# Kernel tuning notes

Hardware: AMD Instinct MI355X
Metric: run time of the kernel (lower is better)

Reference implementation:

```python
import jax, jax.numpy as jnp
import numpy as np


def _conv(h_src, w_e, src, dst, n_dst):
    # u_mul_e('x','w','m') then sum('m','y'): gather src feats, scale by edge weight, segment-sum into dst
    m = h_src[src] * w_e[:, None]  # [E, F]
    return jax.ops.segment_sum(m, dst, num_segments=n_dst)


def setup_inputs() -> dict:
    key = jax.random.key(0)
    ks = jax.random.split(key, 12)
    in_feats, n_hidden, n_classes = 256, 256, 47
    n0, n1, n2, n3 = 100000, 50000, 25000, 12500
    e1, e2, e3 = 800000, 400000, 200000

    def edges(k, e, n_src, n_dst):
        k1, k2, k3 = jax.random.split(k, 3)
        return (jax.random.randint(k1, (e,), 0, n_src, dtype=jnp.int32),
                jax.random.randint(k2, (e,), 0, n_dst, dtype=jnp.int32),
                jax.random.normal(k3, (e,), jnp.float32))

    x = jax.random.normal(ks[0], (n0, in_feats), jnp.float32)
    s1, d1, ew1 = edges(ks[1], e1, n0, n1)
    s2, d2, ew2 = edges(ks[2], e2, n1, n2)
    s3, d3, ew3 = edges(ks[3], e3, n2, n3)
    W1 = jax.random.normal(ks[4], (in_feats, n_hidden), jnp.float32) / np.float32(np.sqrt(in_feats))
    b1 = jnp.zeros((n_hidden,), jnp.float32)
    W2 = jax.random.normal(ks[5], (n_hidden, n_hidden), jnp.float32) / np.float32(np.sqrt(n_hidden))
    b2 = jnp.zeros((n_hidden,), jnp.float32)
    W3 = jax.random.normal(ks[6], (n_hidden, n_classes), jnp.float32) / np.float32(np.sqrt(n_hidden))
    b3 = jnp.zeros((n_classes,), jnp.float32)
    u_sum = jax.random.normal(ks[7], (n2,), jnp.float32)  # per-src-node scalar on last block
    return dict(x=x, W1=W1, b1=b1, W2=W2, b2=b2, W3=W3, b3=b3,
                ew1=ew1, ew2=ew2, ew3=ew3, u_sum=u_sum,
                s1=s1, d1=d1, s2=s2, d2=d2, s3=s3, d3=d3,
                n1=n1, n2=n2, n3=n3)


def reference(x, W1, b1, W2, b2, W3, b3, ew1, ew2, ew3, u_sum,
              s1, d1, s2, d2, s3, d3, n1, n2, n3):
    # layer 1: GraphConv + relu
    h = x @ W1 + b1
    y = jax.nn.relu(_conv(h, ew1, s1, d1, n1))
    # layer 2: GraphConv + relu
    h = y @ W2 + b2
    y = jax.nn.relu(_conv(h, ew2, s2, d2, n2))
    # layer 3: GraphConvReg (no relu on last layer)
    h = y @ W3 + b3  # src feats of last block, [n2, n_classes]
    y = _conv(h, ew3, s3, d3, n3)  # [n3, n_classes]
    mean_x = jnp.mean(y, axis=0)  # [n_classes]
    mean_u = u_sum / jnp.asarray(n3, h.dtype)  # [n2]
    diff = mean_u[:, None] * h - mean_x
    reg_loss = jnp.sum(diff * diff) / (h.shape[0] * h.shape[1])
    return (y, reg_loss)
```

## Files before the change

### kernel.cpp

```cpp
#include <hip/hip_runtime.h>

typedef unsigned int uint;
typedef __attribute__((ext_vector_type(8))) short bf16x8;
typedef __attribute__((ext_vector_type(4))) float f32x4;

__device__ __forceinline__ float b2f(ushort h) { return __uint_as_float(((uint)h) << 16); }
__device__ __forceinline__ ushort f2b(float f) {
    uint u = __float_as_uint(f);
    return (ushort)((u + 0x7fffu + ((u >> 16) & 1u)) >> 16);
}

__global__ __launch_bounds__(256) void zero_i(int* __restrict__ p, int n) {
    int i = blockIdx.x * 256 + threadIdx.x;
    int st = gridDim.x * 256;
    for (; i < n; i += st) p[i] = 0;
}

__global__ __launch_bounds__(1024) void prep_k(
    const float* __restrict__ x, ushort* __restrict__ xb, long n8,
    const float* __restrict__ W1, const float* __restrict__ W2,
    const float* __restrict__ W3, const float* __restrict__ b3,
    ushort* __restrict__ Wt1, ushort* __restrict__ Wt2,
    ushort* __restrict__ Wt3, float* __restrict__ b3p, int NC,
    const int* __restrict__ d1, const int* __restrict__ d2, const int* __restrict__ d3,
    int E1, int E2, int E3, int n1, int n2,
    int* __restrict__ cnt, int* __restrict__ slot, int Gf2b, int NSLOT) {
    int b = blockIdx.x;
    if (b < Gf2b) {
        long i = (long)b * 1024 + threadIdx.x;
        long st = (long)Gf2b * 1024;
        for (; i < n8; i += st) {
            float4 a = reinterpret_cast<const float4*>(x)[i * 2];
            float4 c = reinterpret_cast<const float4*>(x)[i * 2 + 1];
            ushort4 o0, o1;
            o0.x = f2b(a.x); o0.y = f2b(a.y); o0.z = f2b(a.z); o0.w = f2b(a.w);
            o1.x = f2b(c.x); o1.y = f2b(c.y); o1.z = f2b(c.z); o1.w = f2b(c.w);
            reinterpret_cast<ushort4*>(xb)[i * 2] = o0;
            reinterpret_cast<ushort4*>(xb)[i * 2 + 1] = o1;
        }
        return;
    }
    b -= Gf2b;
    if (b < 256) {
        int k = b;
        int t = threadIdx.x;
        if (t < 256) {
            Wt1[(long)t * 256 + k] = f2b(W1[(long)k * 256 + t]);
        } else if (t < 512) {
            int n = t - 256;
            Wt2[(long)n * 256 + k] = f2b(W2[(long)k * 256 + n]);
        } else if (t < 640) {
            int n = t - 512;
            float v = (n < NC) ? W3[(long)k * NC + n] : 0.f;
            Wt3[(long)n * 256 + k] = f2b(v);
            if (k == 0) b3p[n] = (n < NC) ? b3[n] : 0.f;
        }
        return;
    }
    b -= 256;
    const int tid0 = b * 1024 + threadIdx.x;
    const int st = NSLOT * 1024;
    {
        int n4 = E1 >> 2;
        const int4* dd = (const int4*)d1;
        for (int i = tid0; i < n4; i += st) {
            int4 v = dd[i];
            slot[i * 4 + 0] = atomicAdd(&cnt[v.x], 1);
            slot[i * 4 + 1] = atomicAdd(&cnt[v.y], 1);
            slot[i * 4 + 2] = atomicAdd(&cnt[v.z], 1);
            slot[i * 4 + 3] = atomicAdd(&cnt[v.w], 1);
        }
        for (int i = n4 * 4 + tid0; i < E1; i += st) slot[i] = atomicAdd(&cnt[d1[i]], 1);
    }
    {
        int n4 = E2 >> 2;
        const int4* dd = (const int4*)d2;
        int* sl = slot + E1;
        for (int i = tid0; i < n4; i += st) {
            int4 v = dd[i];
            sl[i * 4 + 0] = atomicAdd(&cnt[n1 + v.x], 1);
            sl[i * 4 + 1] = atomicAdd(&cnt[n1 + v.y], 1);
            sl[i * 4 + 2] = atomicAdd(&cnt[n1 + v.z], 1);
            sl[i * 4 + 3] = atomicAdd(&cnt[n1 + v.w], 1);
        }
        for (int i = n4 * 4 + tid0; i < E2; i += st) sl[i] = atomicAdd(&cnt[n1 + d2[i]], 1);
    }
    {
        int n4 = E3 >> 2;
        const int4* dd = (const int4*)d3;
        int* sl = slot + E1 + E2;
        int base = n1 + n2;
        for (int i = tid0; i < n4; i += st) {
            int4 v = dd[i];
            sl[i * 4 + 0] = atomicAdd(&cnt[base + v.x], 1);
            sl[i * 4 + 1] = atomicAdd(&cnt[base + v.y], 1);
            sl[i * 4 + 2] = atomicAdd(&cnt[base + v.z], 1);
            sl[i * 4 + 3] = atomicAdd(&cnt[base + v.w], 1);
        }
        for (int i = n4 * 4 + tid0; i < E3; i += st) sl[i] = atomicAdd(&cnt[base + d3[i]], 1);
    }
}

__global__ __launch_bounds__(1024) void scan1(const int* __restrict__ cnt, int* __restrict__ off,
                                              int* __restrict__ bsum, int n) {
    __shared__ int wsum[16];
    const int lane = threadIdx.x & 63;
    const int wid = threadIdx.x >> 6;
    int i = blockIdx.x * 1024 + threadIdx.x;
    int v = (i < n) ? cnt[i] : 0;
    int s = v;
    #pragma unroll
    for (int o = 1; o < 64; o <<= 1) {
        int t = __shfl_up(s, o, 64);
        if (lane >= o) s += t;
    }
    if (lane == 63) wsum[wid] = s;
    __syncthreads();
    if (wid == 0 && lane < 16) {
        int t = wsum[lane];
        #pragma unroll
        for (int o = 1; o < 16; o <<= 1) {
            int u = __shfl_up(t, o, 64);
            if (lane >= o) t += u;
        }
        wsum[lane] = t;
    }
    __syncthreads();
    int woff = (wid > 0) ? wsum[wid - 1] : 0;
    if (i < n) off[i] = woff + s - v;
    if (threadIdx.x == 0) bsum[blockIdx.x] = wsum[15];
}

__global__ __launch_bounds__(128) void scan2(const int* __restrict__ bsum, int* __restrict__ bbase,
                                             int nb, int* __restrict__ off_end, float* __restrict__ acc) {
    __shared__ int w0tot;
    int tid = threadIdx.x;
    int lane = tid & 63;
    int wid = tid >> 6;
    int v = (tid < nb) ? bsum[tid] : 0;
    int s = v;
    #pragma unroll
    for (int o = 1; o < 64; o <<= 1) {
        int t = __shfl_up(s, o, 64);
        if (lane >= o) s += t;
    }
    if (wid == 0 && lane == 63) w0tot = s;
    __syncthreads();
    int base = (wid == 1) ? w0tot : 0;
    if (tid < nb) bbase[tid] = base + s - v;
    if (tid == nb - 1) *off_end = base + s;
    if (tid == 0) *acc = 0.f;
}

__global__ __launch_bounds__(256) void scan3(int* __restrict__ off, const int* __restrict__ bbase, int n) {
    int i = blockIdx.x * 256 + threadIdx.x;
    int st = gridDim.x * 256;
    for (; i < n; i += st) off[i] += bbase[i >> 10];
}

__global__ __launch_bounds__(256) void place_k(
    const int* __restrict__ s1, const int* __restrict__ d1,
    const int* __restrict__ s2, const int* __restrict__ d2,
    const int* __restrict__ s3, const int* __restrict__ d3,
    const float* __restrict__ w1, const float* __restrict__ w2, const float* __restrict__ w3,
    const int* __restrict__ slot, const int* __restrict__ off,
    int2* __restrict__ csr, int E1, int E2, int E3, int n1, int n2) {
    const int tid0 = blockIdx.x * 256 + threadIdx.x;
    const int st = gridDim.x * 256;
    {
        int n4 = E1 >> 2;
        for (int i = tid0; i < n4; i += st) {
            int4 dv = ((const int4*)d1)[i];
            int4 sv = ((const int4*)s1)[i];
            int4 pv = ((const int4*)slot)[i];
            float4 wv = ((const float4*)w1)[i];
            csr[off[dv.x] + pv.x] = make_int2(sv.x, __float_as_int(wv.x));
            csr[off[dv.y] + pv.y] = make_int2(sv.y, __float_as_int(wv.y));
            csr[off[dv.z] + pv.z] = make_int2(sv.z, __float_as_int(wv.z));
            csr[off[dv.w] + pv.w] = make_int2(sv.w, __float_as_int(wv.w));
        }
        for (int i = n4 * 4 + tid0; i < E1; i += st)
            csr[off[d1[i]] + slot[i]] = make_int2(s1[i], __float_as_int(w1[i]));
    }
    {
        int n4 = E2 >> 2;
        const int* sl = slot + E1;
        for (int i = tid0; i < n4; i += st) {
            int4 dv = ((const int4*)d2)[i];
            int4 sv = ((const int4*)s2)[i];
            int4 pv = ((const int4*)sl)[i];
            float4 wv = ((const float4*)w2)[i];
            csr[off[n1 + dv.x] + pv.x] = make_int2(sv.x, __float_as_int(wv.x));
            csr[off[n1 + dv.y] + pv.y] = make_int2(sv.y, __float_as_int(wv.y));
            csr[off[n1 + dv.z] + pv.z] = make_int2(sv.z, __float_as_int(wv.z));
            csr[off[n1 + dv.w] + pv.w] = make_int2(sv.w, __float_as_int(wv.w));
        }
        for (int i = n4 * 4 + tid0; i < E2; i += st)
            csr[off[n1 + d2[i]] + sl[i]] = make_int2(s2[i], __float_as_int(w2[i]));
    }
    {
        int n4 = E3 >> 2;
        const int* sl = slot + E1 + E2;
        int base = n1 + n2;
        for (int i = tid0; i < n4; i += st) {
            int4 dv = ((const int4*)d3)[i];
            int4 sv = ((const int4*)s3)[i];
            int4 pv = ((const int4*)sl)[i];
            float4 wv = ((const float4*)w3)[i];
            csr[off[base + dv.x] + pv.x] = make_int2(sv.x, __float_as_int(wv.x));
            csr[off[base + dv.y] + pv.y] = make_int2(sv.y, __float_as_int(wv.y));
            csr[off[base + dv.z] + pv.z] = make_int2(sv.z, __float_as_int(wv.z));
            csr[off[base + dv.w] + pv.w] = make_int2(sv.w, __float_as_int(wv.w));
        }
        for (int i = n4 * 4 + tid0; i < E3; i += st)
            csr[off[base + d3[i]] + sl[i]] = make_int2(s3[i], __float_as_int(w3[i]));
    }
}

__global__ __launch_bounds__(256) void gather_b4(const ushort* __restrict__ hb,
                                                 const int* __restrict__ off,
                                                 const int2* __restrict__ csr,
                                                 ushort* __restrict__ out,
                                                 float* __restrict__ rw, int n_dst) {
    int d = blockIdx.x * 4 + (threadIdx.x >> 6);
    if (d >= n_dst) return;
    int lane = threadIdx.x & 63;
    int i0 = off[d], i1 = off[d + 1];
    float a0 = 0.f, a1 = 0.f, a2 = 0.f, a3 = 0.f, sw = 0.f;
    for (int base = i0; base < i1; base += 64) {
        int cnt = i1 - base;
        if (cnt > 64) cnt = 64;
        int2 e = csr[base + (lane < cnt ? lane : 0)];
        int j = 0;
        for (; j + 8 <= cnt; j += 8) {
            int s[8]; float wv[8];
            #pragma unroll
            for (int u = 0; u < 8; ++u) {
                s[u] = __shfl(e.x, j + u, 64);
                wv[u] = __int_as_float(__shfl(e.y, j + u, 64));
            }
            ushort4 v[8];
            #pragma unroll
            for (int u = 0; u < 8; ++u)
                v[u] = *reinterpret_cast<const ushort4*>(&hb[(long)s[u] * 256 + lane * 4]);
            #pragma unroll
            for (int u = 0; u < 8; ++u) {
                a0 += wv[u] * b2f(v[u].x);
                a1 += wv[u] * b2f(v[u].y);
                a2 += wv[u] * b2f(v[u].z);
                a3 += wv[u] * b2f(v[u].w);
                sw += wv[u];
            }
        }
        for (; j < cnt; ++j) {
            int sv = __shfl(e.x, j, 64);
            float wv = __int_as_float(__shfl(e.y, j, 64));
            ushort4 v = *reinterpret_cast<const ushort4*>(&hb[(long)sv * 256 + lane * 4]);
            a0 += wv * b2f(v.x); a1 += wv * b2f(v.y); a2 += wv * b2f(v.z); a3 += wv * b2f(v.w);
            sw += wv;
        }
    }
    ushort4 o;
    o.x = f2b(a0); o.y = f2b(a1); o.z = f2b(a2); o.w = f2b(a3);
    *reinterpret_cast<ushort4*>(&out[(long)d * 256 + lane * 4]) = o;
    if (lane == 0) rw[d] = sw;
}

__global__ __launch_bounds__(256) void gather_small(const float* __restrict__ h,
                                                    const int* __restrict__ off,
                                                    const int2* __restrict__ csr,
                                                    float* __restrict__ y, int n_dst, int F) {
    int d = blockIdx.x * 4 + (threadIdx.x >> 6);
    if (d >= n_dst) return;
    int lane = threadIdx.x & 63;
    int i0 = off[d], i1 = off[d + 1];
    float acc = 0.f;
    for (int base = i0; base < i1; base += 64) {
        int cnt = i1 - base;
        if (cnt > 64) cnt = 64;
        int2 e = csr[base + (lane < cnt ? lane : 0)];
        int j = 0;
        for (; j + 4 <= cnt; j += 4) {
            int s[4]; float wv[4];
            #pragma unroll
            for (int u = 0; u < 4; ++u) {
                s[u] = __shfl(e.x, j + u, 64);
                wv[u] = __int_as_float(__shfl(e.y, j + u, 64));
            }
            float v[4];
            #pragma unroll
            for (int u = 0; u < 4; ++u) v[u] = (lane < F) ? h[(long)s[u] * F + lane] : 0.f;
            #pragma unroll
            for (int u = 0; u < 4; ++u) acc += wv[u] * v[u];
        }
        for (; j < cnt; ++j) {
            int sv = __shfl(e.x, j, 64);
            float wv = __int_as_float(__shfl(e.y, j, 64));
            if (lane < F) acc += wv * h[(long)sv * F + lane];
        }
    }
    if (lane < F) y[(long)d * F + lane] = acc;
}

template <bool RELU, bool OUTF32, bool ROWSC, bool GUARDN>
__global__ __launch_bounds__(256) void gemm_mfma(const ushort* __restrict__ A,
                                                 const ushort* __restrict__ Bt,
                                                 const float* __restrict__ bias,
                                                 const float* __restrict__ rowsc,
                                                 ushort* __restrict__ Cb,
                                                 float* __restrict__ Cf,
                                                 int M, int Nout, int K) {
    __shared__ ushort As[4096];
    __shared__ ushort Bs[4096];
    const int tid = threadIdx.x;
    const int w = tid >> 6;
    const int lane = tid & 63;
    const int l15 = lane & 15;
    const int l4 = lane >> 4;
    const int bm = blockIdx.x * 128;
    const int bn = blockIdx.y * 128;
    const int wm = w >> 1, wn = w & 1;

    int ra0 = bm + w * 16 + l15;       if (ra0 >= M) ra0 = M - 1;
    int ra1 = bm + (w + 4) * 16 + l15; if (ra1 >= M) ra1 = M - 1;
    const ushort* pa0 = A + (long)ra0 * K + l4 * 8;
    const ushort* pa1 = A + (long)ra1 * K + l4 * 8;
    const ushort* pb0 = Bt + (long)(bn + w * 16 + l15) * K + l4 * 8;
    const ushort* pb1 = Bt + (long)(bn + (w + 4) * 16 + l15) * K + l4 * 8;

    f32x4 acc[4][4];
    f32x4 zz = {0.f, 0.f, 0.f, 0.f};
    #pragma unroll
    for (int m = 0; m < 4; ++m)
        #pragma unroll
        for (int n = 0; n < 4; ++n) acc[m][n] = zz;

    for (int k0 = 0; k0 < K; k0 += 32) {
        __builtin_amdgcn_global_load_lds((const __attribute__((address_space(1))) void*)pa0,
                                         (__attribute__((address_space(3))) void*)&As[w * 512], 16, 0, 0);
        __builtin_amdgcn_global_load_lds((const __attribute__((address_space(1))) void*)pa1,
                                         (__attribute__((address_space(3))) void*)&As[(w + 4) * 512], 16, 0, 0);
        __builtin_amdgcn_global_load_lds((const __attribute__((address_space(1))) void*)pb0,
                                         (__attribute__((address_space(3))) void*)&Bs[w * 512], 16, 0, 0);
        __builtin_amdgcn_global_load_lds((const __attribute__((address_space(1))) void*)pb1,
                                         (__attribute__((address_space(3))) void*)&Bs[(w + 4) * 512], 16, 0, 0);
        pa0 += 32; pa1 += 32; pb0 += 32; pb1 += 32;
        __syncthreads();
        bf16x8 af[4], bfr[4];
        #pragma unroll
        for (int m = 0; m < 4; ++m)
            af[m] = *reinterpret_cast<const bf16x8*>(&As[(wm * 4 + m) * 512 + lane * 8]);
        #pragma unroll
        for (int n = 0; n < 4; ++n)
            bfr[n] = *reinterpret_cast<const bf16x8*>(&Bs[(wn * 4 + n) * 512 + lane * 8]);
        #pragma unroll
        for (int m = 0; m < 4; ++m)
            #pragma unroll
            for (int n = 0; n < 4; ++n)
                acc[m][n] = __builtin_amdgcn_mfma_f32_16x16x32_bf16(af[m], bfr[n], acc[m][n], 0, 0, 0);
        __syncthreads();
    }

    const int rbase = bm + wm * 64;
    const int cbase = bn + wn * 64;
    #pragma unroll
    for (int m = 0; m < 4; ++m) {
        #pragma unroll
        for (int q = 0; q < 4; ++q) {
            int r = rbase + m * 16 + l4 * 4 + q;
            if (r >= M) continue;
            float rs = ROWSC ? rowsc[r] : 1.f;
            #pragma unroll
            for (int n = 0; n < 4; ++n) {
                int c = cbase + n * 16 + l15;
                float v = acc[m][n][q] + rs * bias[c];
                if (RELU) v = fmaxf(v, 0.f);
                if (!GUARDN || c < Nout) {
                    if (OUTF32) Cf[(long)r * Nout + c] = v;
                    else Cb[(long)r * Nout + c] = f2b(v);
                }
            }
        }
    }
}

__global__ __launch_bounds__(256) void col_mean(const float* __restrict__ y,
                                                float* __restrict__ mean_x,
                                                int rows, int cols) {
    int j = blockIdx.x;
    float s = 0.f;
    for (int i = threadIdx.x; i < rows; i += blockDim.x) s += y[(long)i * cols + j];
    __shared__ float red[256];
    red[threadIdx.x] = s;
    __syncthreads();
    for (int o = 128; o > 0; o >>= 1) {
        if (threadIdx.x < o) red[threadIdx.x] += red[threadIdx.x + o];
        __syncthreads();
    }
    if (threadIdx.x == 0) mean_x[j] = red[0] / (float)rows;
}

__global__ __launch_bounds__(256) void reg_loss_k(const float* __restrict__ h,
                                                  const float* __restrict__ u_sum,
                                                  const float* __restrict__ mean_x,
                                                  float* __restrict__ acc,
                                                  int rows, int cols, float inv_n3) {
    long total = (long)rows * cols;
    long idx = (long)blockIdx.x * blockDim.x + threadIdx.x;
    long stride = (long)gridDim.x * blockDim.x;
    float s = 0.f;
    for (long t = idx; t < total; t += stride) {
        int i = (int)(t / cols);
        int j = (int)(t - (long)i * cols);
        float mu = u_sum[i] * inv_n3;
        float d = mu * h[t] - mean_x[j];
        s += d * d;
    }
    __shared__ float red[256];
    red[threadIdx.x] = s;
    __syncthreads();
    for (int o = 128; o > 0; o >>= 1) {
        if (threadIdx.x < o) red[threadIdx.x] += red[threadIdx.x + o];
        __syncthreads();
    }
    if (threadIdx.x == 0) atomicAdd(acc, red[0]);
}

__global__ void finalize_k(float* __restrict__ out, const float* __restrict__ acc, float scale) {
    if (threadIdx.x == 0) *out = *acc * scale;
}

extern "C" void kernel_launch(void* const* d_in, const int* in_sizes, int n_in,
                              void* d_out, int out_size, void* d_ws, size_t ws_size,
                              hipStream_t stream) {
    const float* x   = (const float*)d_in[0];
    const float* W1  = (const float*)d_in[1];
    const float* b1  = (const float*)d_in[2];
    const float* W2  = (const float*)d_in[3];
    const float* b2  = (const float*)d_in[4];
    const float* W3  = (const float*)d_in[5];
    const float* b3  = (const float*)d_in[6];
    const float* ew1 = (const float*)d_in[7];
    const float* ew2 = (const float*)d_in[8];
    const float* ew3 = (const float*)d_in[9];
    const float* u_sum = (const float*)d_in[10];
    const int* s1 = (const int*)d_in[11];
    const int* d1 = (const int*)d_in[12];
    const int* s2 = (const int*)d_in[13];
    const int* d2 = (const int*)d_in[14];
    const int* s3 = (const int*)d_in[15];
    const int* d3 = (const int*)d_in[16];

    const int K  = 256;
    const int n0 = in_sizes[0] / K;
    const int E1 = in_sizes[7];
    const int E2 = in_sizes[8];
    const int E3 = in_sizes[9];
    const int n2 = in_sizes[10];
    const int NC = in_sizes[5] / K;
    const int n3 = (out_size - 1) / NC;
    const int n1 = 50000;

    const int NT = n1 + n2 + n3;
    const int Et = E1 + E2 + E3;
    const int nb = (NT + 1023) / 1024;
    const int Gf2b = 1024;
    const int NSLOT = 2048;

    float* ws = (float*)d_ws;
    long o = 0;
    auto take = [&](long words) { float* p = ws + o; o += (words + 3) & ~3L; return p; };
    int*    off  = (int*)take(NT + 1);
    int*    cnt  = (int*)take(NT);
    float*  rw   = take(n1 + n2);
    int*    bsum = (int*)take(nb);
    int*    bbase= (int*)take(nb);
    int*    slot = (int*)take(Et);
    int2*   csr  = (int2*)take(2L * Et);
    ushort* Wt1b = (ushort*)take(256 * 256 / 2);
    ushort* Wt2b = (ushort*)take(256 * 256 / 2);
    ushort* Wt3b = (ushort*)take(128 * 256 / 2);
    float*  b3p  = take(128);
    ushort* aggb = (ushort*)take((long)n1 * 256 / 2);
    ushort* xb   = (ushort*)take((long)n0 * 256 / 2);
    float*  h3   = take((long)n2 * NC);
    float*  mean_x = take(64);
    float*  accs   = take(4);

    ushort* y1b = xb;
    ushort* y2b = xb + (long)n1 * 256;
    float*  rw1 = rw;
    float*  rw2 = rw + n1;

    float* y3   = (float*)d_out;
    float* loss = y3 + (long)n3 * NC;

    dim3 blk(256);

    zero_i<<<dim3(128), blk, 0, stream>>>(cnt, NT);
    prep_k<<<dim3(Gf2b + 256 + NSLOT), dim3(1024), 0, stream>>>(
        x, xb, (long)n0 * 256 / 8,
        W1, W2, W3, b3, Wt1b, Wt2b, Wt3b, b3p, NC,
        d1, d2, d3, E1, E2, E3, n1, n2, cnt, slot, Gf2b, NSLOT);

    scan1<<<dim3(nb), dim3(1024), 0, stream>>>(cnt, off, bsum, NT);
    scan2<<<dim3(1), dim3(128), 0, stream>>>(bsum, bbase, nb, &off[NT], accs);
    scan3<<<dim3(128), blk, 0, stream>>>(off, bbase, NT);
    place_k<<<dim3(2048), blk, 0, stream>>>(s1, d1, s2, d2, s3, d3, ew1, ew2, ew3,
                                            slot, off, csr, E1, E2, E3, n1, n2);

    gather_b4<<<dim3((n1 + 3) / 4), blk, 0, stream>>>(xb, off, csr, aggb, rw1, n1);
    gemm_mfma<true, false, true, false><<<dim3((n1 + 127) / 128, 2), blk, 0, stream>>>(
        aggb, Wt1b, b1, rw1, y1b, nullptr, n1, 256, K);

    gather_b4<<<dim3((n2 + 3) / 4), blk, 0, stream>>>(y1b, off + n1, csr, aggb, rw2, n2);
    gemm_mfma<true, false, true, false><<<dim3((n2 + 127) / 128, 2), blk, 0, stream>>>(
        aggb, Wt2b, b2, rw2, y2b, nullptr, n2, 256, K);

    gemm_mfma<false, true, false, true><<<dim3((n2 + 127) / 128, 1), blk, 0, stream>>>(
        y2b, Wt3b, b3p, nullptr, nullptr, h3, n2, NC, K);
    gather_small<<<dim3((n3 + 3) / 4), blk, 0, stream>>>(h3, off + n1 + n2, csr, y3, n3, NC);

    col_mean<<<dim3(NC), blk, 0, stream>>>(y3, mean_x, n3, NC);
    reg_loss_k<<<dim3(512), blk, 0, stream>>>(h3, u_sum, mean_x, accs, n2, NC, 1.0f / (float)n3);
    finalize_k<<<dim3(1), dim3(1), 0, stream>>>(loss, accs, 1.0f / ((float)n2 * (float)NC));
}
```

Before: 347.3 us.

## Replace global-atomic CSR build with two-pass LDS bucket sort by destination

The old path counted edges per destination with global atomics and then scattered them into CSR order. The new path is a two-level counting sort. Each block first builds a shared-memory histogram over 64-node buckets, the per-block counts are scanned, edges are scattered into bucket order, and each bucket is then sorted locally to produce offsets and CSR entries. This removes contended global atomics and the zeroing kernel, at the cost of an extra pass and an extra temporary buffer. It also adds a 4-way unrolled tail loop to the bf16 gather.

```diff
diff --git a/kernel.cpp b/kernel.cpp
--- a/kernel.cpp
+++ b/kernel.cpp
@@ -10,11 +10,7 @@
     return (ushort)((u + 0x7fffu + ((u >> 16) & 1u)) >> 16);
 }
 
-__global__ __launch_bounds__(256) void zero_i(int* __restrict__ p, int n) {
-    int i = blockIdx.x * 256 + threadIdx.x;
-    int st = gridDim.x * 256;
-    for (; i < n; i += st) p[i] = 0;
-}
+#define NBLK_S 256
 
 __global__ __launch_bounds__(1024) void prep_k(
     const float* __restrict__ x, ushort* __restrict__ xb, long n8,
@@ -24,7 +20,8 @@
     ushort* __restrict__ Wt3, float* __restrict__ b3p, int NC,
     const int* __restrict__ d1, const int* __restrict__ d2, const int* __restrict__ d3,
     int E1, int E2, int E3, int n1, int n2,
-    int* __restrict__ cnt, int* __restrict__ slot, int Gf2b, int NSLOT) {
+    int* __restrict__ bh, int NBKT, int chunk, int Gf2b) {
+    __shared__ int hist[2048];
     int b = blockIdx.x;
     if (b < Gf2b) {
         long i = (long)b * 1024 + threadIdx.x;
@@ -58,47 +55,20 @@
         return;
     }
     b -= 256;
-    const int tid0 = b * 1024 + threadIdx.x;
-    const int st = NSLOT * 1024;
-    {
-        int n4 = E1 >> 2;
-        const int4* dd = (const int4*)d1;
-        for (int i = tid0; i < n4; i += st) {
-            int4 v = dd[i];
-            slot[i * 4 + 0] = atomicAdd(&cnt[v.x], 1);
-            slot[i * 4 + 1] = atomicAdd(&cnt[v.y], 1);
-            slot[i * 4 + 2] = atomicAdd(&cnt[v.z], 1);
-            slot[i * 4 + 3] = atomicAdd(&cnt[v.w], 1);
-        }
-        for (int i = n4 * 4 + tid0; i < E1; i += st) slot[i] = atomicAdd(&cnt[d1[i]], 1);
-    }
-    {
-        int n4 = E2 >> 2;
-        const int4* dd = (const int4*)d2;
-        int* sl = slot + E1;
-        for (int i = tid0; i < n4; i += st) {
-            int4 v = dd[i];
-            sl[i * 4 + 0] = atomicAdd(&cnt[n1 + v.x], 1);
-            sl[i * 4 + 1] = atomicAdd(&cnt[n1 + v.y], 1);
-            sl[i * 4 + 2] = atomicAdd(&cnt[n1 + v.z], 1);
-            sl[i * 4 + 3] = atomicAdd(&cnt[n1 + v.w], 1);
-        }
-        for (int i = n4 * 4 + tid0; i < E2; i += st) sl[i] = atomicAdd(&cnt[n1 + d2[i]], 1);
-    }
-    {
-        int n4 = E3 >> 2;
-        const int4* dd = (const int4*)d3;
-        int* sl = slot + E1 + E2;
-        int base = n1 + n2;
-        for (int i = tid0; i < n4; i += st) {
-            int4 v = dd[i];
-            sl[i * 4 + 0] = atomicAdd(&cnt[base + v.x], 1);
-            sl[i * 4 + 1] = atomicAdd(&cnt[base + v.y], 1);
-            sl[i * 4 + 2] = atomicAdd(&cnt[base + v.z], 1);
-            sl[i * 4 + 3] = atomicAdd(&cnt[base + v.w], 1);
-        }
-        for (int i = n4 * 4 + tid0; i < E3; i += st) sl[i] = atomicAdd(&cnt[base + d3[i]], 1);
-    }
+    const int Et = E1 + E2 + E3;
+    const int c0 = b * chunk;
+    const int c1 = (c0 + chunk < Et) ? c0 + chunk : Et;
+    for (int i = threadIdx.x; i < NBKT; i += 1024) hist[i] = 0;
+    __syncthreads();
+    for (int i = c0 + (int)threadIdx.x; i < c1; i += 1024) {
+        int g;
+        if (i < E1) g = d1[i];
+        else if (i < E1 + E2) g = n1 + d2[i - E1];
+        else g = n1 + n2 + d3[i - E1 - E2];
+        atomicAdd(&hist[g >> 6], 1);
+    }
+    __syncthreads();
+    for (int k = threadIdx.x; k < NBKT; k += 1024) bh[k * NBLK_S + b] = hist[k];
 }
 
 __global__ __launch_bounds__(1024) void scan1(const int* __restrict__ cnt, int* __restrict__ off,
@@ -131,89 +101,103 @@
     if (threadIdx.x == 0) bsum[blockIdx.x] = wsum[15];
 }
 
-__global__ __launch_bounds__(128) void scan2(const int* __restrict__ bsum, int* __restrict__ bbase,
-                                             int nb, int* __restrict__ off_end, float* __restrict__ acc) {
-    __shared__ int w0tot;
+__global__ __launch_bounds__(1024) void scan2b(const int* __restrict__ bsum, int* __restrict__ bbase,
+                                               int n, int* __restrict__ offNT, float* __restrict__ acc) {
+    __shared__ int wsum[16];
     int tid = threadIdx.x;
     int lane = tid & 63;
     int wid = tid >> 6;
-    int v = (tid < nb) ? bsum[tid] : 0;
+    int v = (tid < n) ? bsum[tid] : 0;
     int s = v;
     #pragma unroll
     for (int o = 1; o < 64; o <<= 1) {
         int t = __shfl_up(s, o, 64);
         if (lane >= o) s += t;
     }
-    if (wid == 0 && lane == 63) w0tot = s;
-    __syncthreads();
-    int base = (wid == 1) ? w0tot : 0;
-    if (tid < nb) bbase[tid] = base + s - v;
-    if (tid == nb - 1) *off_end = base + s;
+    if (lane == 63) wsum[wid] = s;
+    __syncthreads();
+    if (wid == 0 && lane < 16) {
+        int t = wsum[lane];
+        #pragma unroll
+        for (int o = 1; o < 16; o <<= 1) {
+            int u = __shfl_up(t, o, 64);
+            if (lane >= o) t += u;
+        }
+        wsum[lane] = t;
+    }
+    __syncthreads();
+    int base = (wid > 0) ? wsum[wid - 1] : 0;
+    int excl = base + s - v;
+    if (tid < n) bbase[tid] = excl;
+    if (tid == n - 1) *offNT = excl + v;
     if (tid == 0) *acc = 0.f;
 }
 
-__global__ __launch_bounds__(256) void scan3(int* __restrict__ off, const int* __restrict__ bbase, int n) {
+__global__ __launch_bounds__(256) void scan3(int* __restrict__ a, const int* __restrict__ bbase, int n) {
     int i = blockIdx.x * 256 + threadIdx.x;
     int st = gridDim.x * 256;
-    for (; i < n; i += st) off[i] += bbase[i >> 10];
-}
-
-__global__ __launch_bounds__(256) void place_k(
+    for (; i < n; i += st) a[i] += bbase[i >> 10];
+}
+
+__global__ __launch_bounds__(1024) void sortC(
     const int* __restrict__ s1, const int* __restrict__ d1,
     const int* __restrict__ s2, const int* __restrict__ d2,
     const int* __restrict__ s3, const int* __restrict__ d3,
     const float* __restrict__ w1, const float* __restrict__ w2, const float* __restrict__ w3,
-    const int* __restrict__ slot, const int* __restrict__ off,
-    int2* __restrict__ csr, int E1, int E2, int E3, int n1, int n2) {
-    const int tid0 = blockIdx.x * 256 + threadIdx.x;
-    const int st = gridDim.x * 256;
-    {
-        int n4 = E1 >> 2;
-        for (int i = tid0; i < n4; i += st) {
-            int4 dv = ((const int4*)d1)[i];
-            int4 sv = ((const int4*)s1)[i];
-            int4 pv = ((const int4*)slot)[i];
-            float4 wv = ((const float4*)w1)[i];
-            csr[off[dv.x] + pv.x] = make_int2(sv.x, __float_as_int(wv.x));
-            csr[off[dv.y] + pv.y] = make_int2(sv.y, __float_as_int(wv.y));
-            csr[off[dv.z] + pv.z] = make_int2(sv.z, __float_as_int(wv.z));
-            csr[off[dv.w] + pv.w] = make_int2(sv.w, __float_as_int(wv.w));
-        }
-        for (int i = n4 * 4 + tid0; i < E1; i += st)
-            csr[off[d1[i]] + slot[i]] = make_int2(s1[i], __float_as_int(w1[i]));
-    }
-    {
-        int n4 = E2 >> 2;
-        const int* sl = slot + E1;
-        for (int i = tid0; i < n4; i += st) {
-            int4 dv = ((const int4*)d2)[i];
-            int4 sv = ((const int4*)s2)[i];
-            int4 pv = ((const int4*)sl)[i];
-            float4 wv = ((const float4*)w2)[i];
-            csr[off[n1 + dv.x] + pv.x] = make_int2(sv.x, __float_as_int(wv.x));
-            csr[off[n1 + dv.y] + pv.y] = make_int2(sv.y, __float_as_int(wv.y));
-            csr[off[n1 + dv.z] + pv.z] = make_int2(sv.z, __float_as_int(wv.z));
-            csr[off[n1 + dv.w] + pv.w] = make_int2(sv.w, __float_as_int(wv.w));
-        }
-        for (int i = n4 * 4 + tid0; i < E2; i += st)
-            csr[off[n1 + d2[i]] + sl[i]] = make_int2(s2[i], __float_as_int(w2[i]));
-    }
-    {
-        int n4 = E3 >> 2;
-        const int* sl = slot + E1 + E2;
-        int base = n1 + n2;
-        for (int i = tid0; i < n4; i += st) {
-            int4 dv = ((const int4*)d3)[i];
-            int4 sv = ((const int4*)s3)[i];
-            int4 pv = ((const int4*)sl)[i];
-            float4 wv = ((const float4*)w3)[i];
-            csr[off[base + dv.x] + pv.x] = make_int2(sv.x, __float_as_int(wv.x));
-            csr[off[base + dv.y] + pv.y] = make_int2(sv.y, __float_as_int(wv.y));
-            csr[off[base + dv.z] + pv.z] = make_int2(sv.z, __float_as_int(wv.z));
-            csr[off[base + dv.w] + pv.w] = make_int2(sv.w, __float_as_int(wv.w));
-        }
-        for (int i = n4 * 4 + tid0; i < E3; i += st)
-            csr[off[base + d3[i]] + sl[i]] = make_int2(s3[i], __float_as_int(w3[i]));
+    const int* __restrict__ bhs, int* __restrict__ bs_g, int2* __restrict__ bs_sw,
+    int E1, int E2, int E3, int n1, int n2, int NBKT, int chunk) {
+    __shared__ int cur[2048];
+    const int b = blockIdx.x;
+    const int Et = E1 + E2 + E3;
+    const int c0 = b * chunk;
+    const int c1 = (c0 + chunk < Et) ? c0 + chunk : Et;
+    for (int k = threadIdx.x; k < NBKT; k += 1024) cur[k] = bhs[k * NBLK_S + b];
+    __syncthreads();
+    for (int i = c0 + (int)threadIdx.x; i < c1; i += 1024) {
+        int g, s, w;
+        if (i < E1) { g = d1[i]; s = s1[i]; w = __float_as_int(w1[i]); }
+        else if (i < E1 + E2) { int j = i - E1; g = n1 + d2[j]; s = s2[j]; w = __float_as_int(w2[j]); }
+        else { int j = i - E1 - E2; g = n1 + n2 + d3[j]; s = s3[j]; w = __float_as_int(w3[j]); }
+        int p = atomicAdd(&cur[g >> 6], 1);
+        bs_g[p] = g;
+        bs_sw[p] = make_int2(s, w);
+    }
+}
+
+__global__ __launch_bounds__(256) void sortD(const int* __restrict__ bhs,
+                                             const int* __restrict__ bs_g,
+                                             const int2* __restrict__ bs_sw,
+                                             int* __restrict__ off, int2* __restrict__ csr,
+                                             int NBKT, int NT, int Et) {
+    __shared__ int hist[64];
+    __shared__ int cur[64];
+    const int b = blockIdx.x;
+    const int g0 = b << 6;
+    const int B0 = bhs[b * NBLK_S];
+    const int B1 = (b == NBKT - 1) ? Et : bhs[(b + 1) * NBLK_S];
+    const int tid = threadIdx.x;
+    if (tid < 64) hist[tid] = 0;
+    __syncthreads();
+    for (int p = B0 + tid; p < B1; p += 256) atomicAdd(&hist[bs_g[p] - g0], 1);
+    __syncthreads();
+    if (tid < 64) {
+        int v = hist[tid];
+        int s = v;
+        #pragma unroll
+        for (int o = 1; o < 64; o <<= 1) {
+            int t = __shfl_up(s, o, 64);
+            if (tid >= o) s += t;
+        }
+        int excl = B0 + s - v;
+        cur[tid] = excl;
+        int g = g0 + tid;
+        if (g < NT) off[g] = excl;
+    }
+    __syncthreads();
+    for (int p = B0 + tid; p < B1; p += 256) {
+        int r = bs_g[p] - g0;
+        int q = atomicAdd(&cur[r], 1);
+        csr[q] = bs_sw[p];
     }
 }
 
@@ -245,6 +229,26 @@
                 v[u] = *reinterpret_cast<const ushort4*>(&hb[(long)s[u] * 256 + lane * 4]);
             #pragma unroll
             for (int u = 0; u < 8; ++u) {
+                a0 += wv[u] * b2f(v[u].x);
+                a1 += wv[u] * b2f(v[u].y);
+                a2 += wv[u] * b2f(v[u].z);
+                a3 += wv[u] * b2f(v[u].w);
+                sw += wv[u];
+            }
+        }
+        for (; j + 4 <= cnt; j += 4) {
+            int s[4]; float wv[4];
+            #pragma unroll
+            for (int u = 0; u < 4; ++u) {
+                s[u] = __shfl(e.x, j + u, 64);
+                wv[u] = __int_as_float(__shfl(e.y, j + u, 64));
+            }
+            ushort4 v[4];
+            #pragma unroll
+            for (int u = 0; u < 4; ++u)
+                v[u] = *reinterpret_cast<const ushort4*>(&hb[(long)s[u] * 256 + lane * 4]);
+            #pragma unroll
+            for (int u = 0; u < 4; ++u) {
                 a0 += wv[u] * b2f(v[u].x);
                 a1 += wv[u] * b2f(v[u].y);
                 a2 += wv[u] * b2f(v[u].z);
@@ -463,20 +467,24 @@
 
     const int NT = n1 + n2 + n3;
     const int Et = E1 + E2 + E3;
-    const int nb = (NT + 1023) / 1024;
+    const int NBKT = (NT + 63) >> 6;
+    const int nscan = NBKT * NBLK_S;
+    const int nb = (nscan + 1023) / 1024;
+    const int chunk = (Et + NBLK_S - 1) / NBLK_S;
     const int Gf2b = 1024;
-    const int NSLOT = 2048;
 
     float* ws = (float*)d_ws;
     long o = 0;
     auto take = [&](long words) { float* p = ws + o; o += (words + 3) & ~3L; return p; };
     int*    off  = (int*)take(NT + 1);
-    int*    cnt  = (int*)take(NT);
-    float*  rw   = take(n1 + n2);
+    int*    bh   = (int*)take(nscan);
+    int*    bhs  = (int*)take(nscan);
     int*    bsum = (int*)take(nb);
     int*    bbase= (int*)take(nb);
-    int*    slot = (int*)take(Et);
+    int*    bs_g = (int*)take(Et);
+    int2*   bs_sw= (int2*)take(2L * Et);
     int2*   csr  = (int2*)take(2L * Et);
+    float*  rw   = take(n1 + n2);
     ushort* Wt1b = (ushort*)take(256 * 256 / 2);
     ushort* Wt2b = (ushort*)take(256 * 256 / 2);
     ushort* Wt3b = (ushort*)take(128 * 256 / 2);
@@ -497,17 +505,18 @@
 
     dim3 blk(256);
 
-    zero_i<<<dim3(128), blk, 0, stream>>>(cnt, NT);
-    prep_k<<<dim3(Gf2b + 256 + NSLOT), dim3(1024), 0, stream>>>(
+    prep_k<<<dim3(Gf2b + 256 + NBLK_S), dim3(1024), 0, stream>>>(
         x, xb, (long)n0 * 256 / 8,
         W1, W2, W3, b3, Wt1b, Wt2b, Wt3b, b3p, NC,
-        d1, d2, d3, E1, E2, E3, n1, n2, cnt, slot, Gf2b, NSLOT);
-
-    scan1<<<dim3(nb), dim3(1024), 0, stream>>>(cnt, off, bsum, NT);
-    scan2<<<dim3(1), dim3(128), 0, stream>>>(bsum, bbase, nb, &off[NT], accs);
-    scan3<<<dim3(128), blk, 0, stream>>>(off, bbase, NT);
-    place_k<<<dim3(2048), blk, 0, stream>>>(s1, d1, s2, d2, s3, d3, ew1, ew2, ew3,
-                                            slot, off, csr, E1, E2, E3, n1, n2);
+        d1, d2, d3, E1, E2, E3, n1, n2, bh, NBKT, chunk, Gf2b);
+
+    scan1<<<dim3(nb), dim3(1024), 0, stream>>>(bh, bhs, bsum, nscan);
+    scan2b<<<dim3(1), dim3(1024), 0, stream>>>(bsum, bbase, nb, &off[NT], accs);
+    scan3<<<dim3(256), blk, 0, stream>>>(bhs, bbase, nscan);
+
+    sortC<<<dim3(NBLK_S), dim3(1024), 0, stream>>>(s1, d1, s2, d2, s3, d3, ew1, ew2, ew3,
+                                                   bhs, bs_g, bs_sw, E1, E2, E3, n1, n2, NBKT, chunk);
+    sortD<<<dim3(NBKT), blk, 0, stream>>>(bhs, bs_g, bs_sw, off, csr, NBKT, NT, Et);
 
     gather_b4<<<dim3((n1 + 3) / 4), blk, 0, stream>>>(xb, off, csr, aggb, rw1, n1);
     gemm_mfma<true, false, true, false><<<dim3((n1 + 127) / 128, 2), blk, 0, stream>>>(
```

Measured after the change: 295.5 us. 1.18x faster.
